# Optimization experiments

Measured on AMD Instinct MI355X. Metric: run time of the kernel, lower is better.

## Reference

```python
import jax, jax.numpy as jnp
import numpy as np

B, N, C = 16, 1024, 768
D = 512
DEPTH = 4
K = 3
HP = WP = 32
A_EPS = 1e-4
POW_MIN = 1e-20
LN_EPS = 1e-5


def setup_inputs() -> dict:
    key = jax.random.key(0)
    ks = jax.random.split(key, 20)
    inp = {
        "tokens": jax.random.normal(ks[0], (B, N, C), dtype=jnp.float32),
        "in_proj_w": jax.random.normal(ks[1], (C, D), dtype=jnp.float32) * 0.02,
        "in_proj_b": jnp.zeros((D,), dtype=jnp.float32),
        "blk_norm_w": jnp.ones((DEPTH, D), dtype=jnp.float32),
        "blk_norm_b": jnp.zeros((DEPTH, D), dtype=jnp.float32),
        "blk_inp_w": jax.random.normal(ks[2], (DEPTH, D, 2 * D), dtype=jnp.float32) * 0.02,
        "blk_inp_b": jnp.zeros((DEPTH, 2 * D), dtype=jnp.float32),
        "blk_conv_w": jax.random.normal(ks[3], (DEPTH, K, K, 1, D), dtype=jnp.float32) * 0.1,
        "blk_conv_b": jnp.zeros((DEPTH, D), dtype=jnp.float32),
        "blk_a_logit": jax.random.normal(ks[4], (DEPTH, D), dtype=jnp.float32) * 0.1,
        "blk_b": jnp.ones((DEPTH, D), dtype=jnp.float32) + jax.random.normal(ks[5], (DEPTH, D), dtype=jnp.float32) * 0.02,
        "blk_c": jnp.ones((DEPTH, D), dtype=jnp.float32) + jax.random.normal(ks[6], (DEPTH, D), dtype=jnp.float32) * 0.02,
        "blk_d": jnp.ones((DEPTH, D), dtype=jnp.float32) + jax.random.normal(ks[7], (DEPTH, D), dtype=jnp.float32) * 0.02,
        "blk_out_w": jax.random.normal(ks[8], (DEPTH, D, D), dtype=jnp.float32) * 0.02,
        "blk_out_b": jnp.zeros((DEPTH, D), dtype=jnp.float32),
        "out_norm_w": jnp.ones((D,), dtype=jnp.float32),
        "out_norm_b": jnp.zeros((D,), dtype=jnp.float32),
    }
    return inp


def _layernorm(x, w, b):
    mu = jnp.mean(x, axis=-1, keepdims=True)
    var = jnp.var(x, axis=-1, keepdims=True)
    return (x - mu) * jax.lax.rsqrt(var + LN_EPS) * w + b


def _ssm_scan(x, a_logit, bb, cc, dd):
    # x: (B', L, D)   s_t = a s_{t-1} + b x_t ; y_t = c s_t + d x_t  (log-domain cumsum form)
    L = x.shape[1]
    a = jnp.clip(jax.nn.sigmoid(a_logit), A_EPS, 1.0 - A_EPS)
    t = jnp.arange(L, dtype=jnp.float32)
    a_pow = jnp.maximum(jnp.exp(t[:, None] * jnp.log(a)[None, :]), POW_MIN)  # (L, D)
    u = x * bb  # (B', L, D)
    r = jnp.cumsum(u / a_pow[None], axis=1)
    s = r * a_pow[None]
    return s * cc + x * dd


def _scan2d(x, a_logit, bb, cc, dd):
    # x: (B, H, W, D); bidirectional row-major + col-major scans, averaged
    Bb, H, W, Dd = x.shape
    L = H * W
    seq_row = x.reshape(Bb, L, Dd)
    seq_col = jnp.transpose(x, (0, 2, 1, 3)).reshape(Bb, L, Dd)
    seqs = jnp.concatenate([seq_row, seq_col], axis=0)            # (2B, L, D)
    all_seqs = jnp.concatenate([seqs, seqs[:, ::-1]], axis=0)     # (4B, L, D)
    y2 = _ssm_scan(all_seqs, a_logit, bb, cc, dd)
    y_f, y_rev = jnp.split(y2, 2, axis=0)
    y = 0.5 * (y_f + y_rev[:, ::-1])
    y_row, y_col = jnp.split(y, 2, axis=0)
    y_row_map = y_row.reshape(Bb, H, W, Dd)
    y_col_map = jnp.transpose(y_col.reshape(Bb, W, H, Dd), (0, 2, 1, 3))
    return 0.5 * (y_row_map + y_col_map)


def _dwconv_silu(x, kernel, bias):
    # x: (B,H,W,D); kernel: (K,K,1,D) depthwise; SAME padding (odd k)
    y = jax.lax.conv_general_dilated(
        x, kernel, window_strides=(1, 1), padding="SAME",
        feature_group_count=x.shape[-1],
        dimension_numbers=("NHWC", "HWIO", "NHWC"))
    return jax.nn.silu(y + bias)


def _block(x, nw, nb, iw, ib, cw, cb, al, sb, sc, sd, ow, ob):
    h = _layernorm(x, nw, nb)
    xg = h @ iw + ib                      # (B,H,W,2D)
    x_in, gate = jnp.split(xg, 2, axis=-1)
    gate = jax.nn.sigmoid(gate)
    u = _dwconv_silu(x_in, cw, cb)
    y = _scan2d(u, al, sb, sc, sd)
    y = (y * gate) @ ow + ob
    return x + y


def reference(tokens, in_proj_w, in_proj_b, blk_norm_w, blk_norm_b, blk_inp_w,
              blk_inp_b, blk_conv_w, blk_conv_b, blk_a_logit, blk_b, blk_c,
              blk_d, blk_out_w, blk_out_b, out_norm_w, out_norm_b):
    x = tokens @ in_proj_w + in_proj_b          # (B, N, D)
    x = x.reshape(B, HP, WP, D)                 # token grid
    for i in range(DEPTH):
        x = _block(x, blk_norm_w[i], blk_norm_b[i], blk_inp_w[i], blk_inp_b[i],
                   blk_conv_w[i], blk_conv_b[i], blk_a_logit[i], blk_b[i],
                   blk_c[i], blk_d[i], blk_out_w[i], blk_out_b[i])
    x = _layernorm(x, out_norm_w, out_norm_b)
    return jnp.mean(x, axis=(1, 2))             # pooled global vector (B, D)
```

## Files before the change

### kernel.cpp

```cpp
#include <hip/hip_runtime.h>
#include <hip/hip_bf16.h>
#include <math.h>

#define NPOS 16384
#define DD   512
#define PP   ((size_t)NPOS * DD)

typedef __bf16 bf16x8 __attribute__((ext_vector_type(8)));
typedef float  f32x4  __attribute__((ext_vector_type(4)));

__device__ __forceinline__ void gload16(const __bf16* g, __bf16* l) {
  __builtin_amdgcn_global_load_lds((__attribute__((address_space(1))) void*)(g),
                                   (__attribute__((address_space(3))) void*)(l), 16, 0, 0);
}
__device__ __forceinline__ void wait_vm0() { asm volatile("s_waitcnt vmcnt(0)" ::: "memory"); }
__device__ __forceinline__ void wait_vm2() { asm volatile("s_waitcnt vmcnt(2)" ::: "memory"); }
__device__ __forceinline__ void wait_lgkm0() { asm volatile("s_waitcnt lgkmcnt(0)" ::: "memory"); }

__global__ __launch_bounds__(512, 4) void gemm_k(
    const __bf16* __restrict__ A, const __bf16* __restrict__ Bt,
    const float* __restrict__ bias, const float* __restrict__ res,
    float* __restrict__ C0, __bf16* __restrict__ C1, __bf16* __restrict__ C1b,
    int N, int K, int epi)
{
  __shared__ __bf16 SM[3 * 4096 * 2];
  __bf16 (*Asm)[4096] = (__bf16(*)[4096])SM;
  __bf16 (*Bsm)[4096] = (__bf16(*)[4096])(SM + 3 * 4096);

  const int tid  = threadIdx.x;
  const int w    = tid >> 6;
  const int lane = tid & 63;
  const int quad = lane >> 4;
  const int l16  = lane & 15;
  const int wm   = (w >> 2) << 6;
  const int wn   = (w & 3) << 5;

  const int nwg = gridDim.x;
  const int cpx = nwg >> 3;
  const int lin = (blockIdx.x & 7) * cpx + (blockIdx.x >> 3);
  const int nbn = N >> 7;
  const int sh  = (nbn == 8) ? 3 : 2;
  const int mt  = lin >> sh;
  const int ntc = lin & (nbn - 1);
  const int bm  = mt << 7;
  const int bn  = ntc << 7;

  const __bf16* Ab = A  + (size_t)bm * K;
  const __bf16* Bb = Bt + (size_t)bn * K;
  const int nk = K >> 5;

  f32x4 acc[4][2];
  #pragma unroll
  for (int i = 0; i < 4; ++i)
    #pragma unroll
    for (int j = 0; j < 2; ++j) acc[i][j] = (f32x4){0.f, 0.f, 0.f, 0.f};

  #define STG(P, gb, tile, buf) {                                               \
    const int r_ = tid >> 2, c_ = tid & 3;                                      \
    gload16(gb + (size_t)r_ * K + ((tile) << 5) + ((c_ ^ ((r_ >> 1) & 3)) << 3),\
            &P[buf][tid << 3]);                                                 \
  }

  STG(Asm, Ab, 0, 0) STG(Bsm, Bb, 0, 0)
  STG(Asm, Ab, 1, 1) STG(Bsm, Bb, 1, 1)
  wait_vm2();
  __builtin_amdgcn_s_barrier();

  int cur = 0;
  for (int t = 0; t < nk; ++t) {
    const int nx2 = (cur == 0) ? 2 : cur - 1;
    const bool st = (t + 2 < nk);

    if (st) {
      STG(Asm, Ab, t + 2, nx2)
      STG(Bsm, Bb, t + 2, nx2)
    }

    bf16x8 af[4], bfr[2];
    #pragma unroll
    for (int i = 0; i < 4; ++i) {
      const int m = wm + i * 16 + l16;
      af[i] = *(const bf16x8*)(&Asm[cur][m * 32 + ((quad ^ ((m >> 1) & 3)) << 3)]);
    }
    #pragma unroll
    for (int j = 0; j < 2; ++j) {
      const int n = wn + j * 16 + l16;
      bfr[j] = *(const bf16x8*)(&Bsm[cur][n * 32 + ((quad ^ ((n >> 1) & 3)) << 3)]);
    }

    __builtin_amdgcn_s_setprio(1);
    #pragma unroll
    for (int i = 0; i < 4; ++i)
      #pragma unroll
      for (int j = 0; j < 2; ++j)
        acc[i][j] = __builtin_amdgcn_mfma_f32_16x16x32_bf16(af[i], bfr[j], acc[i][j], 0, 0, 0);
    __builtin_amdgcn_s_setprio(0);

    if (st) { wait_vm2(); } else { wait_vm0(); }
    __builtin_amdgcn_s_barrier();
    cur = (cur == 2) ? 0 : cur + 1;
  }
  #undef STG

  if (epi == 1) {
    const bool dosig = (bn >= 512);
    __bf16* dst = dosig ? C1 : C1b;
    const int cb = dosig ? (bn - 512) : bn;
    char* wb = (char*)SM + w * 5120;
    #pragma unroll
    for (int i = 0; i < 4; ++i)
      #pragma unroll
      for (int j = 0; j < 2; ++j) {
        const float bv = bias[bn + wn + j * 16 + l16];
        #pragma unroll
        for (int r = 0; r < 4; ++r) {
          float v = acc[i][j][r] + bv;
          if (dosig) v = 1.f / (1.f + expf(-v));
          *(__bf16*)(wb + (i * 16 + quad * 4 + r) * 80 + (j * 16 + l16) * 2) = (__bf16)v;
        }
      }
    wait_lgkm0();
    #pragma unroll
    for (int s = 0; s < 4; ++s) {
      const int rr = s * 16 + (lane >> 2);
      bf16x8 vv = *(bf16x8*)(wb + rr * 80 + (lane & 3) * 16);
      const int grow = bm + wm + rr;
      *(bf16x8*)(dst + (size_t)grow * 512 + cb + wn + (lane & 3) * 8) = vv;
    }
  } else {
    #pragma unroll
    for (int j = 0; j < 2; ++j) {
      const int col = wn + j * 16 + l16;
      const float bv = bias[bn + col];
      #pragma unroll
      for (int i = 0; i < 4; ++i) {
        const int row0 = bm + wm + i * 16 + quad * 4;
        #pragma unroll
        for (int r = 0; r < 4; ++r) {
          float v = acc[i][j][r] + bv;
          size_t off = (size_t)(row0 + r) * N + bn + col;
          if (epi == 2) v += res[off];
          C0[off] = v;
        }
      }
    }
  }
}

__global__ __launch_bounds__(256) void cvt_k(const float* __restrict__ s, __bf16* __restrict__ d)
{
  size_t i = ((size_t)blockIdx.x * 256 + threadIdx.x) * 8;
  float4 a = *(const float4*)(s + i);
  float4 b = *(const float4*)(s + i + 4);
  bf16x8 v;
  v[0] = (__bf16)a.x; v[1] = (__bf16)a.y; v[2] = (__bf16)a.z; v[3] = (__bf16)a.w;
  v[4] = (__bf16)b.x; v[5] = (__bf16)b.y; v[6] = (__bf16)b.z; v[7] = (__bf16)b.w;
  *(bf16x8*)(d + i) = v;
}

__global__ __launch_bounds__(256) void tr_k(const float* __restrict__ src, __bf16* __restrict__ dst,
                                            int K, int N, size_t sstr, size_t dstr)
{
  __shared__ float t[32][33];
  const float* s = src + blockIdx.z * sstr;
  __bf16* d = dst + blockIdx.z * dstr;
  int n0 = blockIdx.x * 32, k0 = blockIdx.y * 32;
  int tx = threadIdx.x & 31, ty = threadIdx.x >> 5;
  #pragma unroll
  for (int i = 0; i < 4; ++i)
    t[ty + i * 8][tx] = s[(size_t)(k0 + ty + i * 8) * N + n0 + tx];
  __syncthreads();
  #pragma unroll
  for (int i = 0; i < 4; ++i)
    d[(size_t)(n0 + ty + i * 8) * K + k0 + tx] = (__bf16)t[tx][ty + i * 8];
}

__global__ __launch_bounds__(256) void ln_k(const float* __restrict__ x, const float* __restrict__ w,
                                            const float* __restrict__ bv, __bf16* __restrict__ out)
{
  int gw = (blockIdx.x * 256 + threadIdx.x) >> 6;
  int lane = threadIdx.x & 63;
  const float* xp = x + ((size_t)gw << 9) + lane * 8;
  float4 u0 = *(const float4*)xp;
  float4 u1 = *(const float4*)(xp + 4);
  float v[8] = {u0.x,u0.y,u0.z,u0.w,u1.x,u1.y,u1.z,u1.w};
  float s = 0.f;
  #pragma unroll
  for (int j = 0; j < 8; ++j) s += v[j];
  #pragma unroll
  for (int off = 32; off; off >>= 1) s += __shfl_xor(s, off, 64);
  float mu = s * (1.f/512.f);
  float q = 0.f;
  #pragma unroll
  for (int j = 0; j < 8; ++j) { float d = v[j] - mu; q += d*d; }
  #pragma unroll
  for (int off = 32; off; off >>= 1) q += __shfl_xor(q, off, 64);
  float rstd = rsqrtf(q * (1.f/512.f) + 1e-5f);
  int dch = lane * 8;
  float4 w0 = *(const float4*)(w + dch),  w1 = *(const float4*)(w + dch + 4);
  float4 b0 = *(const float4*)(bv + dch), b1 = *(const float4*)(bv + dch + 4);
  float wv[8] = {w0.x,w0.y,w0.z,w0.w,w1.x,w1.y,w1.z,w1.w};
  float bb[8] = {b0.x,b0.y,b0.z,b0.w,b1.x,b1.y,b1.z,b1.w};
  bf16x8 ov;
  #pragma unroll
  for (int j = 0; j < 8; ++j) ov[j] = (__bf16)((v[j] - mu) * rstd * wv[j] + bb[j]);
  *(bf16x8*)(out + ((size_t)gw << 9) + dch) = ov;
}

__device__ __forceinline__ float sig_a(float al) {
  float a = 1.f / (1.f + expf(-al));
  return fminf(fmaxf(a, 1e-4f), 1.f - 1e-4f);
}

#define CST 544

__global__ __launch_bounds__(512, 4) void scan2d_k(
    const __bf16* __restrict__ xin, const float* __restrict__ cw, const float* __restrict__ cb,
    const float* __restrict__ alog, const float* __restrict__ bvec, const float* __restrict__ cvec,
    const float* __restrict__ dvec, const __bf16* __restrict__ gate, __bf16* __restrict__ yo)
{
  __shared__ __bf16 T[32 * CST];
  __shared__ __bf16 Y[32 * CST];
  __shared__ float  S[4][32][16];
  const int tid = threadIdx.x;
  const int bx  = blockIdx.x;
  const int cg  = ((bx & 7) << 2) | (bx >> 3);
  const int b   = blockIdx.y;
  const int ch  = tid & 15;
  const int c0  = tid >> 4;
  const int d   = (cg << 4) + ch;

  const float a   = sig_a(alog[d]);
  const float lna = logf(a);
  const float ia  = 1.f / a;
  const float bb  = bvec[d];
  const float sc  = 0.25f * cvec[d];
  const float dd  = dvec[d];

  const __bf16* ub = xin + ((size_t)b << 19) + (cg << 4);

  #pragma unroll
  for (int i = 0; i < 4; ++i) {
    int f = tid + i * 512;
    int pos = f >> 1, half = f & 1;
    *(bf16x8*)(T + (pos >> 5) * CST + ((pos & 31) << 4) + (half << 3))
        = *(const bf16x8*)(ub + (size_t)pos * 512 + (half << 3));
  }
  float w00 = cw[(0 << 9) + d], w01 = cw[(1 << 9) + d], w02 = cw[(2 << 9) + d];
  float w10 = cw[(3 << 9) + d], w11 = cw[(4 << 9) + d], w12 = cw[(5 << 9) + d];
  float w20 = cw[(6 << 9) + d], w21 = cw[(7 << 9) + d], w22 = cw[(8 << 9) + d];
  const float cbv = cb[d];
  const float A0f = expf((float)(c0 << 5) * lna),        R0f = expf((float)(c0 << 5) * -lna);
  const float A0b = expf((float)((31 - c0) << 5) * lna), R0b = expf((float)((31 - c0) << 5) * -lna);
  __syncthreads();

  {
    const bool up = (c0 > 0);
    const bool dn = (c0 < 31);
    float a0 = 0.f, a1 = 0.f, a2 = 0.f;
    float b0 = up ? (float)T[(c0 - 1) * CST + ch] : 0.f;
    float b1 =      (float)T[c0 * CST + ch];
    float b2 = dn ? (float)T[(c0 + 1) * CST + ch] : 0.f;
    #pragma unroll 4
    for (int ww = 0; ww < 32; ++ww) {
      float e0 = 0.f, e1 = 0.f, e2 = 0.f;
      if (ww < 31) {
        e0 = up ? (float)T[(c0 - 1) * CST + ((ww + 1) << 4) + ch] : 0.f;
        e1 =      (float)T[c0 * CST + ((ww + 1) << 4) + ch];
        e2 = dn ? (float)T[(c0 + 1) * CST + ((ww + 1) << 4) + ch] : 0.f;
      }
      float acc0 = cbv;
      acc0 = fmaf(a0, w00, acc0); acc0 = fmaf(b0, w01, acc0); acc0 = fmaf(e0, w02, acc0);
      acc0 = fmaf(a1, w10, acc0); acc0 = fmaf(b1, w11, acc0); acc0 = fmaf(e1, w12, acc0);
      acc0 = fmaf(a2, w20, acc0); acc0 = fmaf(b2, w21, acc0); acc0 = fmaf(e2, w22, acc0);
      acc0 = acc0 / (1.f + expf(-acc0));
      Y[c0 * CST + (ww << 4) + ch] = (__bf16)acc0;
      a0 = b0; a1 = b1; a2 = b2; b0 = e0; b1 = e1; b2 = e2;
    }
  }
  __syncthreads();

  #define STEP(r_, uu_, apr_, rp_)                                 \
    { float rr_ = (apr_ < 1e-20f) ? 1e20f : rp_;                   \
      r_ = fmaf((uu_) * bb, rr_, r_); }

  {
    float pf = A0f, qf = R0f, pb = A0b, qb = R0b;
    float s0 = 0.f, s1 = 0.f, s2 = 0.f, s3 = 0.f;
    #pragma unroll 4
    for (int j = 0; j < 32; ++j) {
      float urf = (float)Y[c0 * CST + (j << 4) + ch];
      float urb = (float)Y[c0 * CST + ((31 - j) << 4) + ch];
      float ucf = (float)Y[j * CST + (c0 << 4) + ch];
      float ucb = (float)Y[(31 - j) * CST + (c0 << 4) + ch];
      STEP(s0, urf, pf, qf)  STEP(s2, ucf, pf, qf)
      STEP(s1, urb, pb, qb)  STEP(s3, ucb, pb, qb)
      pf *= a; qf *= ia; pb *= a; qb *= ia;
    }
    S[0][c0][ch] = s0; S[1][c0][ch] = s1; S[2][c0][ch] = s2; S[3][c0][ch] = s3;
  }
  __syncthreads();

  if (tid < 64) {
    int arr = tid >> 4, ch2 = tid & 15;
    float run = 0.f;
    if ((arr & 1) == 0) {
      #pragma unroll 4
      for (int cc = 0; cc < 32; ++cc) { float v = S[arr][cc][ch2]; S[arr][cc][ch2] = run; run += v; }
    } else {
      #pragma unroll 4
      for (int cc = 31; cc >= 0; --cc) { float v = S[arr][cc][ch2]; S[arr][cc][ch2] = run; run += v; }
    }
  }
  __syncthreads();

  {
    float r = S[2][c0][ch];
    float p = A0f, q = R0f;
    #pragma unroll 4
    for (int j = 0; j < 32; ++j) {
      int i0 = j * CST + (c0 << 4) + ch;
      float u = (float)Y[i0];
      float ap = fmaxf(p, 1e-20f);
      STEP(r, u, p, q)
      T[i0] = (__bf16)(r * ap);
      p *= a; q *= ia;
    }
  }
  {
    float r = S[3][c0][ch];
    float p = A0b, q = R0b;
    #pragma unroll 4
    for (int j = 31; j >= 0; --j) {
      int i0 = j * CST + (c0 << 4) + ch;
      float u = (float)Y[i0];
      float ap = fmaxf(p, 1e-20f);
      STEP(r, u, p, q)
      T[i0] = (__bf16)(sc * ((float)T[i0] + r * ap));
      p *= a; q *= ia;
    }
  }
  __syncthreads();

  {
    float r = S[0][c0][ch];
    float p = A0f, q = R0f;
    #pragma unroll 4
    for (int j = 0; j < 32; ++j) {
      int i0 = c0 * CST + (j << 4) + ch;
      float u = (float)Y[i0];
      float ap = fmaxf(p, 1e-20f);
      STEP(r, u, p, q)
      T[i0] = (__bf16)((float)T[i0] + sc * (r * ap));
      p *= a; q *= ia;
    }
  }
  {
    const __bf16* gb = gate + ((size_t)b << 19) + (cg << 4) + ch;
    __bf16* yb = yo + ((size_t)b << 19) + (cg << 4) + ch;
    float r = S[1][c0][ch];
    float p = A0b, q = R0b;
    #pragma unroll 4
    for (int j = 31; j >= 0; --j) {
      int pp = (c0 << 5) + j;
      int i0 = c0 * CST + (j << 4) + ch;
      float u = (float)Y[i0];
      float ap = fmaxf(p, 1e-20f);
      STEP(r, u, p, q)
      float y0 = (float)T[i0] + sc * (r * ap) + dd * u;
      yb[(size_t)pp * 512] = (__bf16)(y0 * (float)gb[(size_t)pp * 512]);
      p *= a; q *= ia;
    }
  }
  #undef STEP
}

__global__ __launch_bounds__(256) void reduce_k(const __bf16* __restrict__ hn, float* __restrict__ out)
{
  __shared__ float part[4][64];
  int l = threadIdx.x & 63;
  int q = threadIdx.x >> 6;
  int d = blockIdx.y * 64 + l;
  int b = blockIdx.x;
  const __bf16* p = hn + ((size_t)b << 19) + d + ((size_t)(q * 256) << 9);
  float s0 = 0.f, s1 = 0.f, s2 = 0.f, s3 = 0.f;
  for (int t = 0; t < 256; t += 4) {
    s0 += (float)p[(size_t)(t+0) << 9];
    s1 += (float)p[(size_t)(t+1) << 9];
    s2 += (float)p[(size_t)(t+2) << 9];
    s3 += (float)p[(size_t)(t+3) << 9];
  }
  part[q][l] = (s0 + s1) + (s2 + s3);
  __syncthreads();
  if (threadIdx.x < 64)
    out[b * 512 + d] = (part[0][l] + part[1][l] + part[2][l] + part[3][l]) * (1.f / 1024.f);
}

extern "C" void kernel_launch(void* const* d_in, const int* in_sizes, int n_in,
                              void* d_out, int out_size, void* d_ws, size_t ws_size,
                              hipStream_t stream)
{
  const float* tokens = (const float*)d_in[0];
  const float* in_w   = (const float*)d_in[1];
  const float* in_b   = (const float*)d_in[2];
  const float* nw     = (const float*)d_in[3];
  const float* nb     = (const float*)d_in[4];
  const float* iw     = (const float*)d_in[5];
  const float* ib     = (const float*)d_in[6];
  const float* cw     = (const float*)d_in[7];
  const float* cb     = (const float*)d_in[8];
  const float* al     = (const float*)d_in[9];
  const float* bbv    = (const float*)d_in[10];
  const float* ccv    = (const float*)d_in[11];
  const float* ddv    = (const float*)d_in[12];
  const float* ow     = (const float*)d_in[13];
  const float* obv    = (const float*)d_in[14];
  const float* onw    = (const float*)d_in[15];
  const float* onb    = (const float*)d_in[16];

  float*  x     = (float*)d_ws;
  __bf16* hy16  = (__bf16*)(x + PP);
  __bf16* xin16 = hy16 + PP;
  __bf16* g16   = xin16 + PP;
  __bf16* iwT   = g16 + PP;
  __bf16* owT   = iwT + (size_t)4 * 1024 * 512;
  __bf16* tb16  = owT + (size_t)4 * 512 * 512;
  __bf16* inwT  = xin16;

  cvt_k<<<6144, 256, 0, stream>>>(tokens, tb16);
  tr_k<<<dim3(16, 24, 1), 256, 0, stream>>>(in_w, inwT, 768, 512, 0, 0);
  tr_k<<<dim3(32, 16, 4), 256, 0, stream>>>(iw, iwT, 512, 1024, (size_t)512*1024, (size_t)1024*512);
  tr_k<<<dim3(16, 16, 4), 256, 0, stream>>>(ow, owT, 512, 512, (size_t)512*512, (size_t)512*512);

  gemm_k<<<512, 512, 0, stream>>>(tb16, inwT, in_b, nullptr, x, nullptr, nullptr,
                                  512, 768, 0);

  for (int i = 0; i < 4; ++i) {
    ln_k<<<4096, 256, 0, stream>>>(x, nw + i*512, nb + i*512, hy16);
    gemm_k<<<1024, 512, 0, stream>>>(hy16, iwT + (size_t)i*1024*512, ib + i*1024,
                                     nullptr, nullptr, g16, xin16, 1024, 512, 1);
    scan2d_k<<<dim3(32, 16), 512, 0, stream>>>(xin16, cw + i*9*512, cb + i*512,
                                               al + i*512, bbv + i*512, ccv + i*512,
                                               ddv + i*512, g16, hy16);
    gemm_k<<<512, 512, 0, stream>>>(hy16, owT + (size_t)i*512*512, obv + i*512,
                                    x, x, nullptr, nullptr, 512, 512, 2);
  }

  ln_k<<<4096, 256, 0, stream>>>(x, onw, onb, hy16);
  reduce_k<<<dim3(16, 8), 256, 0, stream>>>(hy16, (float*)d_out);
}
```

Baseline: 535.8 us.

## Load B operand straight to registers in the in-projection GEMM

Adds a templated GEMM variant used for the block input projection. In it, the B (weight) operand fragments are loaded from global memory directly into registers with a register double-buffer, while A still stages through LDS. This removes the B LDS staging and reads, and shrinks shared memory. The cost is redundant global/L2 reads of B across waves and more register pressure, and the wait counts are adjusted to match.

```diff
diff --git a/kernel.cpp b/kernel.cpp
--- a/kernel.cpp
+++ b/kernel.cpp
@@ -15,15 +15,17 @@
 }
 __device__ __forceinline__ void wait_vm0() { asm volatile("s_waitcnt vmcnt(0)" ::: "memory"); }
 __device__ __forceinline__ void wait_vm2() { asm volatile("s_waitcnt vmcnt(2)" ::: "memory"); }
+__device__ __forceinline__ void wait_vm3() { asm volatile("s_waitcnt vmcnt(3)" ::: "memory"); }
 __device__ __forceinline__ void wait_lgkm0() { asm volatile("s_waitcnt lgkmcnt(0)" ::: "memory"); }
 
+template<int BDIR>
 __global__ __launch_bounds__(512, 4) void gemm_k(
     const __bf16* __restrict__ A, const __bf16* __restrict__ Bt,
     const float* __restrict__ bias, const float* __restrict__ res,
     float* __restrict__ C0, __bf16* __restrict__ C1, __bf16* __restrict__ C1b,
     int N, int K, int epi)
 {
-  __shared__ __bf16 SM[3 * 4096 * 2];
+  __shared__ __bf16 SM[BDIR ? 20480 : 24576];
   __bf16 (*Asm)[4096] = (__bf16(*)[4096])SM;
   __bf16 (*Bsm)[4096] = (__bf16(*)[4096])(SM + 3 * 4096);
 
@@ -45,8 +47,10 @@
   const int bm  = mt << 7;
   const int bn  = ntc << 7;
 
-  const __bf16* Ab = A  + (size_t)bm * K;
+  const __bf16* Ab = A + (size_t)bm * K;
   const __bf16* Bb = Bt + (size_t)bn * K;
+  const __bf16* Bp0 = Bt + (size_t)(bn + wn + l16) * K + quad * 8;
+  const __bf16* Bp1 = Bp0 + (size_t)16 * K;
   const int nk = K >> 5;
 
   f32x4 acc[4][2];
@@ -61,44 +65,79 @@
             &P[buf][tid << 3]);                                                 \
   }
 
-  STG(Asm, Ab, 0, 0) STG(Bsm, Bb, 0, 0)
-  STG(Asm, Ab, 1, 1) STG(Bsm, Bb, 1, 1)
-  wait_vm2();
-  __builtin_amdgcn_s_barrier();
-
   int cur = 0;
-  for (int t = 0; t < nk; ++t) {
-    const int nx2 = (cur == 0) ? 2 : cur - 1;
-    const bool st = (t + 2 < nk);
-
-    if (st) {
-      STG(Asm, Ab, t + 2, nx2)
-      STG(Bsm, Bb, t + 2, nx2)
-    }
-
-    bf16x8 af[4], bfr[2];
-    #pragma unroll
-    for (int i = 0; i < 4; ++i) {
-      const int m = wm + i * 16 + l16;
-      af[i] = *(const bf16x8*)(&Asm[cur][m * 32 + ((quad ^ ((m >> 1) & 3)) << 3)]);
-    }
-    #pragma unroll
-    for (int j = 0; j < 2; ++j) {
-      const int n = wn + j * 16 + l16;
-      bfr[j] = *(const bf16x8*)(&Bsm[cur][n * 32 + ((quad ^ ((n >> 1) & 3)) << 3)]);
-    }
-
-    __builtin_amdgcn_s_setprio(1);
-    #pragma unroll
-    for (int i = 0; i < 4; ++i)
-      #pragma unroll
-      for (int j = 0; j < 2; ++j)
-        acc[i][j] = __builtin_amdgcn_mfma_f32_16x16x32_bf16(af[i], bfr[j], acc[i][j], 0, 0, 0);
-    __builtin_amdgcn_s_setprio(0);
-
-    if (st) { wait_vm2(); } else { wait_vm0(); }
+  if constexpr (BDIR == 0) {
+    STG(Asm, Ab, 0, 0) STG(Bsm, Bb, 0, 0)
+    STG(Asm, Ab, 1, 1) STG(Bsm, Bb, 1, 1)
+    wait_vm2();
     __builtin_amdgcn_s_barrier();
-    cur = (cur == 2) ? 0 : cur + 1;
+
+    for (int t = 0; t < nk; ++t) {
+      const int nx2 = (cur == 0) ? 2 : cur - 1;
+      const bool st = (t + 2 < nk);
+      if (st) {
+        STG(Asm, Ab, t + 2, nx2)
+        STG(Bsm, Bb, t + 2, nx2)
+      }
+      bf16x8 af[4], bfr[2];
+      #pragma unroll
+      for (int i = 0; i < 4; ++i) {
+        const int m = wm + i * 16 + l16;
+        af[i] = *(const bf16x8*)(&Asm[cur][m * 32 + ((quad ^ ((m >> 1) & 3)) << 3)]);
+      }
+      #pragma unroll
+      for (int j = 0; j < 2; ++j) {
+        const int n = wn + j * 16 + l16;
+        bfr[j] = *(const bf16x8*)(&Bsm[cur][n * 32 + ((quad ^ ((n >> 1) & 3)) << 3)]);
+      }
+      __builtin_amdgcn_s_setprio(1);
+      #pragma unroll
+      for (int i = 0; i < 4; ++i) {
+        acc[i][0] = __builtin_amdgcn_mfma_f32_16x16x32_bf16(af[i], bfr[0], acc[i][0], 0, 0, 0);
+        acc[i][1] = __builtin_amdgcn_mfma_f32_16x16x32_bf16(af[i], bfr[1], acc[i][1], 0, 0, 0);
+      }
+      __builtin_amdgcn_s_setprio(0);
+      if (st) { wait_vm2(); } else { wait_vm0(); }
+      __builtin_amdgcn_s_barrier();
+      cur = (cur == 2) ? 0 : cur + 1;
+    }
+  } else {
+    STG(Asm, Ab, 0, 0)
+    STG(Asm, Ab, 1, 1)
+    bf16x8 bq0 = *(const bf16x8*)(Bp0);
+    bf16x8 bq1 = *(const bf16x8*)(Bp1);
+    bf16x8 br0 = *(const bf16x8*)(Bp0 + 32);
+    bf16x8 br1 = *(const bf16x8*)(Bp1 + 32);
+    wait_vm0();
+    __builtin_amdgcn_s_barrier();
+
+    for (int t = 0; t < nk; ++t) {
+      const int nx2 = (cur == 0) ? 2 : cur - 1;
+      const bool st = (t + 2 < nk);
+      bf16x8 bs0 = br0, bs1 = br1;
+      if (st) {
+        STG(Asm, Ab, t + 2, nx2)
+        bs0 = *(const bf16x8*)(Bp0 + ((t + 2) << 5));
+        bs1 = *(const bf16x8*)(Bp1 + ((t + 2) << 5));
+      }
+      bf16x8 af[4];
+      #pragma unroll
+      for (int i = 0; i < 4; ++i) {
+        const int m = wm + i * 16 + l16;
+        af[i] = *(const bf16x8*)(&Asm[cur][m * 32 + ((quad ^ ((m >> 1) & 3)) << 3)]);
+      }
+      __builtin_amdgcn_s_setprio(1);
+      #pragma unroll
+      for (int i = 0; i < 4; ++i) {
+        acc[i][0] = __builtin_amdgcn_mfma_f32_16x16x32_bf16(af[i], bq0, acc[i][0], 0, 0, 0);
+        acc[i][1] = __builtin_amdgcn_mfma_f32_16x16x32_bf16(af[i], bq1, acc[i][1], 0, 0, 0);
+      }
+      __builtin_amdgcn_s_setprio(0);
+      if (st) { wait_vm3(); } else if (t + 1 < nk) { wait_vm0(); }
+      __builtin_amdgcn_s_barrier();
+      bq0 = br0; bq1 = br1; br0 = bs0; br1 = bs1;
+      cur = (cur == 2) ? 0 : cur + 1;
+    }
   }
   #undef STG
 
@@ -432,18 +471,18 @@
   tr_k<<<dim3(32, 16, 4), 256, 0, stream>>>(iw, iwT, 512, 1024, (size_t)512*1024, (size_t)1024*512);
   tr_k<<<dim3(16, 16, 4), 256, 0, stream>>>(ow, owT, 512, 512, (size_t)512*512, (size_t)512*512);
 
-  gemm_k<<<512, 512, 0, stream>>>(tb16, inwT, in_b, nullptr, x, nullptr, nullptr,
-                                  512, 768, 0);
+  gemm_k<0><<<512, 512, 0, stream>>>(tb16, inwT, in_b, nullptr, x, nullptr, nullptr,
+                                     512, 768, 0);
 
   for (int i = 0; i < 4; ++i) {
     ln_k<<<4096, 256, 0, stream>>>(x, nw + i*512, nb + i*512, hy16);
-    gemm_k<<<1024, 512, 0, stream>>>(hy16, iwT + (size_t)i*1024*512, ib + i*1024,
-                                     nullptr, nullptr, g16, xin16, 1024, 512, 1);
+    gemm_k<1><<<1024, 512, 0, stream>>>(hy16, iwT + (size_t)i*1024*512, ib + i*1024,
+                                        nullptr, nullptr, g16, xin16, 1024, 512, 1);
     scan2d_k<<<dim3(32, 16), 512, 0, stream>>>(xin16, cw + i*9*512, cb + i*512,
                                                al + i*512, bbv + i*512, ccv + i*512,
                                                ddv + i*512, g16, hy16);
-    gemm_k<<<512, 512, 0, stream>>>(hy16, owT + (size_t)i*512*512, obv + i*512,
-                                    x, x, nullptr, nullptr, 512, 512, 2);
+    gemm_k<0><<<512, 512, 0, stream>>>(hy16, owT + (size_t)i*512*512, obv + i*512,
+                                       x, x, nullptr, nullptr, 512, 512, 2);
   }
 
   ln_k<<<4096, 256, 0, stream>>>(x, onw, onb, hy16);
```

Result: slower. 598.7 us (+11.8%).
